# Performance work log

Measured on AMD Instinct MI355X. Metric: run time of the kernel, lower is better.

The kernel has to match this reference:

```python
import jax, jax.numpy as jnp
import numpy as np

N_USERS = 50000
N_PRODS = 50000
N_NODES = N_USERS + N_PRODS
N_EDGES = 600000
UD, PD, H, O = 64, 100, 128, 16


def _gcn_conv(x, W, b, src, dst, n):
    """PyG GCNConv: linear transform, add self-loops, sym-normalized scatter-add."""
    x = x @ W                                    # [n, H]
    loop = jnp.arange(n, dtype=src.dtype)
    src = jnp.concatenate([src, loop])
    dst = jnp.concatenate([dst, loop])
    deg = jax.ops.segment_sum(jnp.ones_like(dst, dtype=x.dtype), dst, num_segments=n)
    dinv = jnp.where(deg > 0, jax.lax.rsqrt(deg), 0.0)
    norm = dinv[src] * dinv[dst]                 # [E+n]
    msg = x[src] * norm[:, None]                 # gather + scale
    out = jax.ops.segment_sum(msg, dst, num_segments=n)
    return out + b


def setup_inputs() -> dict:
    key = jax.random.key(0)
    ks = jax.random.split(key, 16)
    s = 0.05
    return {
        "user_feats": jax.random.normal(ks[0], (N_USERS, UD), dtype=jnp.float32),
        "prod_feats": jax.random.normal(ks[1], (N_PRODS, PD), dtype=jnp.float32),
        "edge_index": jax.random.randint(ks[2], (2, N_EDGES), 0, N_NODES, dtype=jnp.int64),
        "Wu": jax.random.normal(ks[3], (UD, H), dtype=jnp.float32) * s,
        "bu": jnp.zeros((H,), dtype=jnp.float32),
        "Wp": jax.random.normal(ks[4], (PD, H), dtype=jnp.float32) * s,
        "bp": jnp.zeros((H,), dtype=jnp.float32),
        "W1": jax.random.normal(ks[5], (H, H), dtype=jnp.float32) * s,
        "b1": jnp.zeros((H,), dtype=jnp.float32),
        "W2": jax.random.normal(ks[6], (H, H), dtype=jnp.float32) * s,
        "b2": jnp.zeros((H,), dtype=jnp.float32),
        "W3": jax.random.normal(ks[7], (H, H), dtype=jnp.float32) * s,
        "b3": jnp.zeros((H,), dtype=jnp.float32),
        "Wo": jax.random.normal(ks[8], (H, O), dtype=jnp.float32) * s,
        "bo": jnp.zeros((O,), dtype=jnp.float32),
    }


def reference(user_feats, prod_feats, edge_index, Wu, bu, Wp, bp,
              W1, b1, W2, b2, W3, b3, Wo, bo):
    src, dst = edge_index[0], edge_index[1]
    user_x = user_feats @ Wu + bu
    prod_x = prod_feats @ Wp + bp
    x = jnp.concatenate([user_x, prod_x], axis=0)   # [N_NODES, H]
    x = jax.nn.relu(_gcn_conv(x, W1, b1, src, dst, N_NODES))
    # dropout p=0.6 is identity in eval mode
    x = jax.nn.relu(_gcn_conv(x, W2, b2, src, dst, N_NODES))
    x = jax.nn.relu(_gcn_conv(x, W3, b3, src, dst, N_NODES))
    return x @ Wo + bo                              # [N_NODES, O]
```

## Files before the change

### kernel.cpp

```cpp
#include <hip/hip_runtime.h>
#include <hip/hip_fp16.h>

#define NU 50000
#define NP 50000
#define NN 100000
#define NE 600000
#define H  128
#define O  16

typedef __attribute__((ext_vector_type(8))) _Float16 half8;
typedef __attribute__((ext_vector_type(4))) _Float16 h4v;
typedef __attribute__((ext_vector_type(4))) float f32x4;

__global__ void k_prep(const float* __restrict__ Wu, const float* __restrict__ Wp,
                       const float* __restrict__ W1, const float* __restrict__ W2,
                       const float* __restrict__ W3, const float* __restrict__ Wo,
                       __half* __restrict__ whU, __half* __restrict__ wlU,
                       __half* __restrict__ whP, __half* __restrict__ wlP,
                       __half* __restrict__ wh1, __half* __restrict__ wl1,
                       __half* __restrict__ wh2, __half* __restrict__ wl2,
                       __half* __restrict__ wh3, __half* __restrict__ wl3,
                       __half* __restrict__ whO, __half* __restrict__ wlO,
                       int* __restrict__ cnt) {
    int idx = blockIdx.x * blockDim.x + threadIdx.x;
    if (idx >= 75776) {
        int i = idx - 75776;
        if (i < NN) cnt[i] = 0;
        return;
    }
    const float* W; __half *Wh, *Wl; int K, KPAD, NC;
    if      (idx <  8192) {              W = Wu; Wh = whU; Wl = wlU; K =  64; KPAD =  64; NC = 128; }
    else if (idx < 24576) { idx -=  8192; W = Wp; Wh = whP; Wl = wlP; K = 100; KPAD = 128; NC = 128; }
    else if (idx < 40960) { idx -= 24576; W = W1; Wh = wh1; Wl = wl1; K = 128; KPAD = 128; NC = 128; }
    else if (idx < 57344) { idx -= 40960; W = W2; Wh = wh2; Wl = wl2; K = 128; KPAD = 128; NC = 128; }
    else if (idx < 73728) { idx -= 57344; W = W3; Wh = wh3; Wl = wl3; K = 128; KPAD = 128; NC = 128; }
    else                  { idx -= 73728; W = Wo; Wh = whO; Wl = wlO; K = 128; KPAD = 128; NC =  16; }
    int n = idx / KPAD, k = idx - n * KPAD;
    float x = (k < K) ? W[k * NC + n] * 16.0f : 0.0f;
    __half h = __float2half_rn(x);
    __half l = __float2half_rn(x - __half2float(h));
    Wh[idx] = h; Wl[idx] = l;
}

__global__ void k_count(const int* __restrict__ dst, int* __restrict__ cnt,
                        int* __restrict__ rank, int E) {
    int e = blockIdx.x * blockDim.x + threadIdx.x;
    if (e < E) rank[e] = atomicAdd(&cnt[dst[e]], 1);
}

#define SCAN_TPB 256
#define SCAN_VPT 4
#define SCAN_CHUNK (SCAN_TPB * SCAN_VPT)

__global__ void k_scan1(const int* __restrict__ in, int* __restrict__ out,
                        int* __restrict__ bsums, float* __restrict__ dinv, int n) {
    __shared__ int sh[SCAN_TPB];
    int t = threadIdx.x, b = blockIdx.x;
    int base = b * SCAN_CHUNK + t * SCAN_VPT;
    int v[SCAN_VPT]; int s = 0;
#pragma unroll
    for (int i = 0; i < SCAN_VPT; i++) {
        int idx = base + i;
        v[i] = (idx < n) ? in[idx] : 0;
        if (idx < n) dinv[idx] = rsqrtf((float)(v[i] + 1));
        s += v[i];
    }
    sh[t] = s; __syncthreads();
    for (int off = 1; off < SCAN_TPB; off <<= 1) {
        int x = (t >= off) ? sh[t - off] : 0;
        __syncthreads();
        sh[t] += x;
        __syncthreads();
    }
    int run = (t > 0) ? sh[t - 1] : 0;
    if (t == SCAN_TPB - 1) bsums[b] = sh[t];
#pragma unroll
    for (int i = 0; i < SCAN_VPT; i++) {
        int idx = base + i;
        if (idx < n) out[idx] = run;
        run += v[i];
    }
}

__global__ void k_scan2(int* __restrict__ bsums, int nb) {
    __shared__ int sh[128];
    int t = threadIdx.x;
    int v = (t < nb) ? bsums[t] : 0;
    sh[t] = v; __syncthreads();
    for (int off = 1; off < 128; off <<= 1) {
        int x = (t >= off) ? sh[t - off] : 0;
        __syncthreads();
        sh[t] += x;
        __syncthreads();
    }
    if (t < nb) bsums[t] = sh[t] - v;
}

__global__ void k_fill(const int* __restrict__ src, const int* __restrict__ dst,
                       const int* __restrict__ offs, const int* __restrict__ bsums,
                       const int* __restrict__ rank, const float* __restrict__ dinv,
                       int2* __restrict__ epack, int E) {
    int e = blockIdx.x * blockDim.x + threadIdx.x;
    if (e < E) {
        int s = src[e], d = dst[e];
        int p = offs[d] + bsums[d >> 10] + rank[e];
        int2 r;
        r.x = s;
        r.y = __float_as_int(dinv[s] * dinv[d]);
        epack[p] = r;
    }
}

template <typename AT, int K, int KPAD, int MI, int NOUT, bool BIAS, bool F32OUT>
__device__ __forceinline__
void gemm_body(const AT* __restrict__ X,
               const __half* __restrict__ Wh, const __half* __restrict__ Wl,
               const float* __restrict__ bias, void* __restrict__ Cout,
               int M, int orow0, int vb) {
    constexpr int KS = KPAD / 32;
    const int tid  = threadIdx.x;
    const int wid  = tid >> 6, lane = tid & 63;
    const int lm   = lane & 15, q = lane >> 4;
    const int gw   = vb * 4 + wid;
    const int NT   = (M + 63) >> 6;
    int tile, c0;
    if constexpr (MI == 4) { tile = gw >> 1; c0 = (gw & 1) * 64; }
    else                   { tile = gw;      c0 = 0; }
    if (tile >= NT) return;
    const int n0 = tile * 64;

    half8 wh[MI][KS], wl[MI][KS];
#pragma unroll
    for (int mi = 0; mi < MI; mi++)
#pragma unroll
        for (int ks = 0; ks < KS; ks++) {
            const size_t b = (size_t)(c0 + mi * 16 + lm) * KPAD + ks * 32 + q * 8;
            wh[mi][ks] = *(const half8*)&Wh[b];
            wl[mi][ks] = *(const half8*)&Wl[b];
        }

    f32x4 acc[4][MI];
#pragma unroll
    for (int ni = 0; ni < 4; ni++)
#pragma unroll
        for (int mi = 0; mi < MI; mi++) acc[ni][mi] = (f32x4)0.0f;

#pragma unroll
    for (int ni = 0; ni < 4; ni++) {
        const int node = n0 + ni * 16 + lm;
        half8 xf[KS];
        if (node < M) {
            if constexpr (sizeof(AT) == 2) {
#pragma unroll
                for (int ks = 0; ks < KS; ks++)
                    xf[ks] = *(const half8*)((const __half*)X + (size_t)node * KPAD + ks * 32 + q * 8);
            } else {
                const float* xp = (const float*)X + (size_t)node * K;
#pragma unroll
                for (int ks = 0; ks < KS; ks++) {
                    const int kb = ks * 32 + q * 8;
                    if (kb + 8 <= K) {
                        float4 v0 = *(const float4*)(xp + kb);
                        float4 v1 = *(const float4*)(xp + kb + 4);
                        xf[ks][0] = (_Float16)v0.x; xf[ks][1] = (_Float16)v0.y;
                        xf[ks][2] = (_Float16)v0.z; xf[ks][3] = (_Float16)v0.w;
                        xf[ks][4] = (_Float16)v1.x; xf[ks][5] = (_Float16)v1.y;
                        xf[ks][6] = (_Float16)v1.z; xf[ks][7] = (_Float16)v1.w;
                    } else {
#pragma unroll
                        for (int j = 0; j < 8; j++) {
                            int k = kb + j;
                            xf[ks][j] = (k < K) ? (_Float16)xp[k] : (_Float16)0.0f;
                        }
                    }
                }
            }
        } else {
#pragma unroll
            for (int ks = 0; ks < KS; ks++)
#pragma unroll
                for (int j = 0; j < 8; j++) xf[ks][j] = (_Float16)0.0f;
        }
#pragma unroll
        for (int ks = 0; ks < KS; ks++)
#pragma unroll
            for (int mi = 0; mi < MI; mi++) {
                acc[ni][mi] = __builtin_amdgcn_mfma_f32_16x16x32_f16(wh[mi][ks], xf[ks], acc[ni][mi], 0, 0, 0);
                acc[ni][mi] = __builtin_amdgcn_mfma_f32_16x16x32_f16(wl[mi][ks], xf[ks], acc[ni][mi], 0, 0, 0);
            }
    }

#pragma unroll
    for (int ni = 0; ni < 4; ni++) {
        const int node = n0 + ni * 16 + lm;
        if (node >= M) continue;
#pragma unroll
        for (int mi = 0; mi < MI; mi++) {
            const int cb = c0 + mi * 16 + q * 4;
            float4 bv = BIAS ? *(const float4*)&bias[cb] : make_float4(0.f, 0.f, 0.f, 0.f);
            float v0 = fmaf(acc[ni][mi][0], 0.0625f, bv.x);
            float v1 = fmaf(acc[ni][mi][1], 0.0625f, bv.y);
            float v2 = fmaf(acc[ni][mi][2], 0.0625f, bv.z);
            float v3 = fmaf(acc[ni][mi][3], 0.0625f, bv.w);
            if constexpr (F32OUT) {
                *(float4*)((float*)Cout + (size_t)(orow0 + node) * NOUT + cb) =
                    make_float4(v0, v1, v2, v3);
            } else {
                __half2 h0 = __floats2half2_rn(v0, v1);
                __half2 h1 = __floats2half2_rn(v2, v3);
                uint2 o; o.x = *(unsigned*)&h0; o.y = *(unsigned*)&h1;
                *(uint2*)((__half*)Cout + (size_t)(orow0 + node) * NOUT + cb) = o;
            }
        }
    }
}

template <typename AT, int K, int KPAD, int MI, int NOUT, bool BIAS, bool F32OUT>
__launch_bounds__(256)
__global__ void k_gemm_reg(const AT* __restrict__ X,
                           const __half* __restrict__ Wh, const __half* __restrict__ Wl,
                           const float* __restrict__ bias, void* __restrict__ Cout,
                           int M, int orow0) {
    gemm_body<AT, K, KPAD, MI, NOUT, BIAS, F32OUT>(X, Wh, Wl, bias, Cout, M, orow0, blockIdx.x);
}

__launch_bounds__(256)
__global__ void k_gemm_inputs(const float* __restrict__ user, const float* __restrict__ prod,
                              const __half* __restrict__ whU, const __half* __restrict__ wlU,
                              const __half* __restrict__ whP, const __half* __restrict__ wlP,
                              const float* __restrict__ bu, const float* __restrict__ bp,
                              void* __restrict__ xA, int blkU) {
    if ((int)blockIdx.x < blkU)
        gemm_body<float,  64,  64, 4, 128, true, false>(user, whU, wlU, bu, xA, NU, 0, blockIdx.x);
    else
        gemm_body<float, 100, 128, 4, 128, true, false>(prod, whP, wlP, bp, xA, NP, NU, blockIdx.x - blkU);
}

__launch_bounds__(256)
__global__ void k_aggregate(const __half* __restrict__ y, const int* __restrict__ offs,
                            const int* __restrict__ bsums, const int2* __restrict__ epack,
                            const float* __restrict__ dinv, const float* __restrict__ bias,
                            __half* __restrict__ out) {
    const int node = __builtin_amdgcn_readfirstlane(blockIdx.x * 4 + (threadIdx.x >> 6));
    const int l = threadIdx.x & 63;
    const int h = l >> 5, j = l & 31;

    int e0 = offs[node] + bsums[node >> 10];
    int e1 = (node + 1 < NN) ? (offs[node + 1] + bsums[(node + 1) >> 10]) : NE;
    e0 = __builtin_amdgcn_readfirstlane(e0);
    e1 = __builtin_amdgcn_readfirstlane(e1);

    const h4v* y4 = (const h4v*)y;
    f32x4 acc0 = (f32x4)0.f, acc1 = (f32x4)0.f, acc2 = (f32x4)0.f, acc3 = (f32x4)0.f;
    const int e1m1 = e1 - 1;

    for (int e = e0; e < e1; e += 8) {
        const int ee0 = e + 0 + h;
        const int ee1 = e + 2 + h;
        const int ee2 = e + 4 + h;
        const int ee3 = e + 6 + h;
        int2 p0 = epack[min(ee0, e1m1)];
        int2 p1 = epack[min(ee1, e1m1)];
        int2 p2 = epack[min(ee2, e1m1)];
        int2 p3 = epack[min(ee3, e1m1)];
        float w0 = (ee0 < e1) ? __int_as_float(p0.y) : 0.f;
        float w1 = (ee1 < e1) ? __int_as_float(p1.y) : 0.f;
        float w2 = (ee2 < e1) ? __int_as_float(p2.y) : 0.f;
        float w3 = (ee3 < e1) ? __int_as_float(p3.y) : 0.f;
        h4v v0 = y4[(size_t)p0.x * 32 + j];
        h4v v1 = y4[(size_t)p1.x * 32 + j];
        h4v v2 = y4[(size_t)p2.x * 32 + j];
        h4v v3 = y4[(size_t)p3.x * 32 + j];
        acc0[0] = fmaf((float)v0[0], w0, acc0[0]); acc0[1] = fmaf((float)v0[1], w0, acc0[1]);
        acc0[2] = fmaf((float)v0[2], w0, acc0[2]); acc0[3] = fmaf((float)v0[3], w0, acc0[3]);
        acc1[0] = fmaf((float)v1[0], w1, acc1[0]); acc1[1] = fmaf((float)v1[1], w1, acc1[1]);
        acc1[2] = fmaf((float)v1[2], w1, acc1[2]); acc1[3] = fmaf((float)v1[3], w1, acc1[3]);
        acc2[0] = fmaf((float)v2[0], w2, acc2[0]); acc2[1] = fmaf((float)v2[1], w2, acc2[1]);
        acc2[2] = fmaf((float)v2[2], w2, acc2[2]); acc2[3] = fmaf((float)v2[3], w2, acc2[3]);
        acc3[0] = fmaf((float)v3[0], w3, acc3[0]); acc3[1] = fmaf((float)v3[1], w3, acc3[1]);
        acc3[2] = fmaf((float)v3[2], w3, acc3[2]); acc3[3] = fmaf((float)v3[3], w3, acc3[3]);
    }

    f32x4 s = (acc0 + acc1) + (acc2 + acc3);
    float t0 = s[0] + __shfl_xor(s[0], 32, 64);
    float t1 = s[1] + __shfl_xor(s[1], 32, 64);
    float t2 = s[2] + __shfl_xor(s[2], 32, 64);
    float t3 = s[3] + __shfl_xor(s[3], 32, 64);

    const float di2 = dinv[node] * dinv[node];
    h4v sv = y4[(size_t)node * 32 + j];
    float4 bv = *(const float4*)&bias[4 * j];
    float r0 = fmaf((float)sv[0], di2, t0) + bv.x;
    float r1 = fmaf((float)sv[1], di2, t1) + bv.y;
    float r2 = fmaf((float)sv[2], di2, t2) + bv.z;
    float r3 = fmaf((float)sv[3], di2, t3) + bv.w;
    if (l < 32) {
        __half2 ha = __floats2half2_rn(fmaxf(r0, 0.f), fmaxf(r1, 0.f));
        __half2 hb = __floats2half2_rn(fmaxf(r2, 0.f), fmaxf(r3, 0.f));
        uint2 o; o.x = *(unsigned*)&ha; o.y = *(unsigned*)&hb;
        *(uint2*)(out + (size_t)node * H + 4 * j) = o;
    }
}

extern "C" void kernel_launch(void* const* d_in, const int* in_sizes, int n_in,
                              void* d_out, int out_size, void* d_ws, size_t ws_size,
                              hipStream_t stream) {
    const float* user = (const float*)d_in[0];
    const float* prod = (const float*)d_in[1];
    const int*   eidx = (const int*)  d_in[2];
    const int*   edst = eidx + NE;
    const int*   esrc = eidx;
    const float* Wu = (const float*)d_in[3];
    const float* bu = (const float*)d_in[4];
    const float* Wp = (const float*)d_in[5];
    const float* bp = (const float*)d_in[6];
    const float* W1 = (const float*)d_in[7];
    const float* b1 = (const float*)d_in[8];
    const float* W2 = (const float*)d_in[9];
    const float* b2 = (const float*)d_in[10];
    const float* W3 = (const float*)d_in[11];
    const float* b3 = (const float*)d_in[12];
    const float* Wo = (const float*)d_in[13];
    const float* bo = (const float*)d_in[14];
    float* out = (float*)d_out;

    char* ws = (char*)d_ws;
    size_t p = 0;
    auto alloc = [&](size_t bytes) -> void* {
        void* r = ws + p;
        p += (bytes + 255) & ~(size_t)255;
        return r;
    };
    __half* xA   = (__half*)alloc((size_t)NN * H * 2);
    __half* xB   = (__half*)alloc((size_t)NN * H * 2);
    int*   cnt   = (int*)  alloc((size_t)NN * 4);
    int*   rank  = (int*)  alloc((size_t)NE * 4);
    int*   offs  = (int*)  alloc((size_t)(NN + 1) * 4);
    float* dinv  = (float*)alloc((size_t)NN * 4);
    int2*  epack = (int2*) alloc((size_t)NE * 8);
    int*   bsums = (int*)  alloc(128 * 4);
    __half* whU = (__half*)alloc(128 * 64 * 2);
    __half* wlU = (__half*)alloc(128 * 64 * 2);
    __half* whP = (__half*)alloc(128 * 128 * 2);
    __half* wlP = (__half*)alloc(128 * 128 * 2);
    __half* wh1 = (__half*)alloc(128 * 128 * 2);
    __half* wl1 = (__half*)alloc(128 * 128 * 2);
    __half* wh2 = (__half*)alloc(128 * 128 * 2);
    __half* wl2 = (__half*)alloc(128 * 128 * 2);
    __half* wh3 = (__half*)alloc(128 * 128 * 2);
    __half* wl3 = (__half*)alloc(128 * 128 * 2);
    __half* whO = (__half*)alloc(16 * 128 * 2);
    __half* wlO = (__half*)alloc(16 * 128 * 2);

    const int NBLK = (NN + SCAN_CHUNK - 1) / SCAN_CHUNK;

    k_prep<<<(75776 + NN + 255) / 256, 256, 0, stream>>>(
        Wu, Wp, W1, W2, W3, Wo,
        whU, wlU, whP, wlP, wh1, wl1, wh2, wl2, wh3, wl3, whO, wlO, cnt);

    k_count<<<(NE + 255) / 256, 256, 0, stream>>>(edst, cnt, rank, NE);
    k_scan1<<<NBLK, SCAN_TPB, 0, stream>>>(cnt, offs, bsums, dinv, NN);
    k_scan2<<<1, 128, 0, stream>>>(bsums, NBLK);
    k_fill <<<(NE + 255) / 256, 256, 0, stream>>>(esrc, edst, offs, bsums, rank, dinv,
                                                  epack, NE);

    {
        constexpr int ntU = (NU + 63) / 64, blkU = (ntU * 2 + 3) / 4;
        constexpr int ntP = (NP + 63) / 64, blkP = (ntP * 2 + 3) / 4;
        k_gemm_inputs<<<blkU + blkP, 256, 0, stream>>>(
            user, prod, whU, wlU, whP, wlP, bu, bp, xA, blkU);
    }

    const int ntN  = (NN + 63) / 64;
    const int blkG = (ntN * 2 + 3) / 4;
    const int blkO = (ntN + 3) / 4;

    k_gemm_reg<__half, 128, 128, 4, 128, false, false><<<blkG, 256, 0, stream>>>(xA, wh1, wl1, nullptr, xB, NN, 0);
    k_aggregate<<<NN / 4, 256, 0, stream>>>(xB, offs, bsums, epack, dinv, b1, xA);
    k_gemm_reg<__half, 128, 128, 4, 128, false, false><<<blkG, 256, 0, stream>>>(xA, wh2, wl2, nullptr, xB, NN, 0);
    k_aggregate<<<NN / 4, 256, 0, stream>>>(xB, offs, bsums, epack, dinv, b2, xA);
    k_gemm_reg<__half, 128, 128, 4, 128, false, false><<<blkG, 256, 0, stream>>>(xA, wh3, wl3, nullptr, xB, NN, 0);
    k_aggregate<<<NN / 4, 256, 0, stream>>>(xB, offs, bsums, epack, dinv, b3, xA);

    k_gemm_reg<__half, 128, 128, 1, 16, true, true><<<blkO, 256, 0, stream>>>(xA, whO, wlO, bo, out, NN, 0);
}
```

Baseline: 303.2 us.

## Shrink GEMM tiles to 16 nodes per wave and vectorize aggregate edge loads

The register GEMM now gives each wave 16 nodes instead of 64. Weights are reloaded per k-step from cache rather than held in registers for the whole tile. This cuts register pressure and raises the number of waves in flight, at the cost of more weight loads from L1/L2. The aggregate kernel reads 4 contiguous packed edges per half-wave instead of strided clamped indices. It relies on an 8-entry zero-padded tail in the edge array, initialized in the prep kernel. The self-term and bias loads are hoisted before the edge loop so they overlap with the gathers.

```diff
diff --git a/kernel.cpp b/kernel.cpp
--- a/kernel.cpp
+++ b/kernel.cpp
@@ -21,11 +21,12 @@
                        __half* __restrict__ wh2, __half* __restrict__ wl2,
                        __half* __restrict__ wh3, __half* __restrict__ wl3,
                        __half* __restrict__ whO, __half* __restrict__ wlO,
-                       int* __restrict__ cnt) {
+                       int* __restrict__ cnt, int2* __restrict__ epack) {
     int idx = blockIdx.x * blockDim.x + threadIdx.x;
     if (idx >= 75776) {
         int i = idx - 75776;
         if (i < NN) cnt[i] = 0;
+        else if (i < NN + 8) { int2 z; z.x = 0; z.y = 0; epack[NE + (i - NN)] = z; }
         return;
     }
     const float* W; __half *Wh, *Wl; int K, KPAD, NC;
@@ -118,99 +119,87 @@
                const float* __restrict__ bias, void* __restrict__ Cout,
                int M, int orow0, int vb) {
     constexpr int KS = KPAD / 32;
+    constexpr int CSPLIT = NOUT / (16 * MI);
     const int tid  = threadIdx.x;
     const int wid  = tid >> 6, lane = tid & 63;
     const int lm   = lane & 15, q = lane >> 4;
     const int gw   = vb * 4 + wid;
-    const int NT   = (M + 63) >> 6;
-    int tile, c0;
-    if constexpr (MI == 4) { tile = gw >> 1; c0 = (gw & 1) * 64; }
-    else                   { tile = gw;      c0 = 0; }
-    if (tile >= NT) return;
-    const int n0 = tile * 64;
-
-    half8 wh[MI][KS], wl[MI][KS];
-#pragma unroll
-    for (int mi = 0; mi < MI; mi++)
-#pragma unroll
-        for (int ks = 0; ks < KS; ks++) {
-            const size_t b = (size_t)(c0 + mi * 16 + lm) * KPAD + ks * 32 + q * 8;
-            wh[mi][ks] = *(const half8*)&Wh[b];
-            wl[mi][ks] = *(const half8*)&Wl[b];
-        }
-
-    f32x4 acc[4][MI];
-#pragma unroll
-    for (int ni = 0; ni < 4; ni++)
-#pragma unroll
-        for (int mi = 0; mi < MI; mi++) acc[ni][mi] = (f32x4)0.0f;
-
-#pragma unroll
-    for (int ni = 0; ni < 4; ni++) {
-        const int node = n0 + ni * 16 + lm;
-        half8 xf[KS];
-        if (node < M) {
-            if constexpr (sizeof(AT) == 2) {
-#pragma unroll
-                for (int ks = 0; ks < KS; ks++)
-                    xf[ks] = *(const half8*)((const __half*)X + (size_t)node * KPAD + ks * 32 + q * 8);
-            } else {
-                const float* xp = (const float*)X + (size_t)node * K;
-#pragma unroll
-                for (int ks = 0; ks < KS; ks++) {
-                    const int kb = ks * 32 + q * 8;
-                    if (kb + 8 <= K) {
-                        float4 v0 = *(const float4*)(xp + kb);
-                        float4 v1 = *(const float4*)(xp + kb + 4);
-                        xf[ks][0] = (_Float16)v0.x; xf[ks][1] = (_Float16)v0.y;
-                        xf[ks][2] = (_Float16)v0.z; xf[ks][3] = (_Float16)v0.w;
-                        xf[ks][4] = (_Float16)v1.x; xf[ks][5] = (_Float16)v1.y;
-                        xf[ks][6] = (_Float16)v1.z; xf[ks][7] = (_Float16)v1.w;
-                    } else {
-#pragma unroll
-                        for (int j = 0; j < 8; j++) {
-                            int k = kb + j;
-                            xf[ks][j] = (k < K) ? (_Float16)xp[k] : (_Float16)0.0f;
-                        }
-                    }
+    const int ng   = gw / CSPLIT;
+    const int c0   = (gw % CSPLIT) * (MI * 16);
+    const int NT16 = (M + 15) >> 4;
+    if (ng >= NT16) return;
+    const int node = ng * 16 + lm;
+
+    half8 xf[KS];
+    if (node < M) {
+        if constexpr (sizeof(AT) == 2) {
+#pragma unroll
+            for (int ks = 0; ks < KS; ks++)
+                xf[ks] = *(const half8*)((const __half*)X + (size_t)node * KPAD + ks * 32 + q * 8);
+        } else {
+            const float* xp = (const float*)X + (size_t)node * K;
+#pragma unroll
+            for (int ks = 0; ks < KS; ks++) {
+                const int kb = ks * 32 + q * 8;
+                if (kb + 8 <= K) {
+                    float4 v0 = *(const float4*)(xp + kb);
+                    float4 v1 = *(const float4*)(xp + kb + 4);
+                    xf[ks][0] = (_Float16)v0.x; xf[ks][1] = (_Float16)v0.y;
+                    xf[ks][2] = (_Float16)v0.z; xf[ks][3] = (_Float16)v0.w;
+                    xf[ks][4] = (_Float16)v1.x; xf[ks][5] = (_Float16)v1.y;
+                    xf[ks][6] = (_Float16)v1.z; xf[ks][7] = (_Float16)v1.w;
+                } else if (kb + 4 <= K) {
+                    float4 v0 = *(const float4*)(xp + kb);
+                    xf[ks][0] = (_Float16)v0.x; xf[ks][1] = (_Float16)v0.y;
+                    xf[ks][2] = (_Float16)v0.z; xf[ks][3] = (_Float16)v0.w;
+                    xf[ks][4] = (_Float16)0.0f; xf[ks][5] = (_Float16)0.0f;
+                    xf[ks][6] = (_Float16)0.0f; xf[ks][7] = (_Float16)0.0f;
+                } else {
+#pragma unroll
+                    for (int j = 0; j < 8; j++) xf[ks][j] = (_Float16)0.0f;
                 }
             }
+        }
+    } else {
+#pragma unroll
+        for (int ks = 0; ks < KS; ks++)
+#pragma unroll
+            for (int j = 0; j < 8; j++) xf[ks][j] = (_Float16)0.0f;
+    }
+
+    f32x4 acc[MI];
+#pragma unroll
+    for (int mi = 0; mi < MI; mi++) acc[mi] = (f32x4)0.0f;
+
+#pragma unroll
+    for (int ks = 0; ks < KS; ks++) {
+#pragma unroll
+        for (int mi = 0; mi < MI; mi++) {
+            const size_t b = (size_t)(c0 + mi * 16 + lm) * KPAD + ks * 32 + q * 8;
+            half8 wh = *(const half8*)&Wh[b];
+            half8 wl = *(const half8*)&Wl[b];
+            acc[mi] = __builtin_amdgcn_mfma_f32_16x16x32_f16(wh, xf[ks], acc[mi], 0, 0, 0);
+            acc[mi] = __builtin_amdgcn_mfma_f32_16x16x32_f16(wl, xf[ks], acc[mi], 0, 0, 0);
+        }
+    }
+
+    if (node >= M) return;
+#pragma unroll
+    for (int mi = 0; mi < MI; mi++) {
+        const int cb = c0 + mi * 16 + q * 4;
+        float4 bv = BIAS ? *(const float4*)&bias[cb] : make_float4(0.f, 0.f, 0.f, 0.f);
+        float v0 = fmaf(acc[mi][0], 0.0625f, bv.x);
+        float v1 = fmaf(acc[mi][1], 0.0625f, bv.y);
+        float v2 = fmaf(acc[mi][2], 0.0625f, bv.z);
+        float v3 = fmaf(acc[mi][3], 0.0625f, bv.w);
+        if constexpr (F32OUT) {
+            *(float4*)((float*)Cout + (size_t)(orow0 + node) * NOUT + cb) =
+                make_float4(v0, v1, v2, v3);
         } else {
-#pragma unroll
-            for (int ks = 0; ks < KS; ks++)
-#pragma unroll
-                for (int j = 0; j < 8; j++) xf[ks][j] = (_Float16)0.0f;
-        }
-#pragma unroll
-        for (int ks = 0; ks < KS; ks++)
-#pragma unroll
-            for (int mi = 0; mi < MI; mi++) {
-                acc[ni][mi] = __builtin_amdgcn_mfma_f32_16x16x32_f16(wh[mi][ks], xf[ks], acc[ni][mi], 0, 0, 0);
-                acc[ni][mi] = __builtin_amdgcn_mfma_f32_16x16x32_f16(wl[mi][ks], xf[ks], acc[ni][mi], 0, 0, 0);
-            }
-    }
-
-#pragma unroll
-    for (int ni = 0; ni < 4; ni++) {
-        const int node = n0 + ni * 16 + lm;
-        if (node >= M) continue;
-#pragma unroll
-        for (int mi = 0; mi < MI; mi++) {
-            const int cb = c0 + mi * 16 + q * 4;
-            float4 bv = BIAS ? *(const float4*)&bias[cb] : make_float4(0.f, 0.f, 0.f, 0.f);
-            float v0 = fmaf(acc[ni][mi][0], 0.0625f, bv.x);
-            float v1 = fmaf(acc[ni][mi][1], 0.0625f, bv.y);
-            float v2 = fmaf(acc[ni][mi][2], 0.0625f, bv.z);
-            float v3 = fmaf(acc[ni][mi][3], 0.0625f, bv.w);
-            if constexpr (F32OUT) {
-                *(float4*)((float*)Cout + (size_t)(orow0 + node) * NOUT + cb) =
-                    make_float4(v0, v1, v2, v3);
-            } else {
-                __half2 h0 = __floats2half2_rn(v0, v1);
-                __half2 h1 = __floats2half2_rn(v2, v3);
-                uint2 o; o.x = *(unsigned*)&h0; o.y = *(unsigned*)&h1;
-                *(uint2*)((__half*)Cout + (size_t)(orow0 + node) * NOUT + cb) = o;
-            }
+            __half2 h0 = __floats2half2_rn(v0, v1);
+            __half2 h1 = __floats2half2_rn(v2, v3);
+            uint2 o; o.x = *(unsigned*)&h0; o.y = *(unsigned*)&h1;
+            *(uint2*)((__half*)Cout + (size_t)(orow0 + node) * NOUT + cb) = o;
         }
     }
 }
@@ -251,22 +240,24 @@
     e1 = __builtin_amdgcn_readfirstlane(e1);
 
     const h4v* y4 = (const h4v*)y;
+
+    const float di2 = dinv[node] * dinv[node];
+    h4v sv = y4[(size_t)node * 32 + j];
+    float4 bv = *(const float4*)&bias[4 * j];
+
     f32x4 acc0 = (f32x4)0.f, acc1 = (f32x4)0.f, acc2 = (f32x4)0.f, acc3 = (f32x4)0.f;
-    const int e1m1 = e1 - 1;
 
     for (int e = e0; e < e1; e += 8) {
-        const int ee0 = e + 0 + h;
-        const int ee1 = e + 2 + h;
-        const int ee2 = e + 4 + h;
-        const int ee3 = e + 6 + h;
-        int2 p0 = epack[min(ee0, e1m1)];
-        int2 p1 = epack[min(ee1, e1m1)];
-        int2 p2 = epack[min(ee2, e1m1)];
-        int2 p3 = epack[min(ee3, e1m1)];
-        float w0 = (ee0 < e1) ? __int_as_float(p0.y) : 0.f;
-        float w1 = (ee1 < e1) ? __int_as_float(p1.y) : 0.f;
-        float w2 = (ee2 < e1) ? __int_as_float(p2.y) : 0.f;
-        float w3 = (ee3 < e1) ? __int_as_float(p3.y) : 0.f;
+        const int eb = e + 4 * h;
+        const int2* pe = epack + eb;
+        int2 p0 = pe[0];
+        int2 p1 = pe[1];
+        int2 p2 = pe[2];
+        int2 p3 = pe[3];
+        float w0 = (eb + 0 < e1) ? __int_as_float(p0.y) : 0.f;
+        float w1 = (eb + 1 < e1) ? __int_as_float(p1.y) : 0.f;
+        float w2 = (eb + 2 < e1) ? __int_as_float(p2.y) : 0.f;
+        float w3 = (eb + 3 < e1) ? __int_as_float(p3.y) : 0.f;
         h4v v0 = y4[(size_t)p0.x * 32 + j];
         h4v v1 = y4[(size_t)p1.x * 32 + j];
         h4v v2 = y4[(size_t)p2.x * 32 + j];
@@ -287,9 +278,6 @@
     float t2 = s[2] + __shfl_xor(s[2], 32, 64);
     float t3 = s[3] + __shfl_xor(s[3], 32, 64);
 
-    const float di2 = dinv[node] * dinv[node];
-    h4v sv = y4[(size_t)node * 32 + j];
-    float4 bv = *(const float4*)&bias[4 * j];
     float r0 = fmaf((float)sv[0], di2, t0) + bv.x;
     float r1 = fmaf((float)sv[1], di2, t1) + bv.y;
     float r2 = fmaf((float)sv[2], di2, t2) + bv.z;
@@ -337,7 +325,7 @@
     int*   rank  = (int*)  alloc((size_t)NE * 4);
     int*   offs  = (int*)  alloc((size_t)(NN + 1) * 4);
     float* dinv  = (float*)alloc((size_t)NN * 4);
-    int2*  epack = (int2*) alloc((size_t)NE * 8);
+    int2*  epack = (int2*) alloc((size_t)(NE + 8) * 8);
     int*   bsums = (int*)  alloc(128 * 4);
     __half* whU = (__half*)alloc(128 * 64 * 2);
     __half* wlU = (__half*)alloc(128 * 64 * 2);
@@ -354,9 +342,9 @@
 
     const int NBLK = (NN + SCAN_CHUNK - 1) / SCAN_CHUNK;
 
-    k_prep<<<(75776 + NN + 255) / 256, 256, 0, stream>>>(
+    k_prep<<<(75776 + NN + 8 + 255) / 256, 256, 0, stream>>>(
         Wu, Wp, W1, W2, W3, Wo,
-        whU, wlU, whP, wlP, wh1, wl1, wh2, wl2, wh3, wl3, whO, wlO, cnt);
+        whU, wlU, whP, wlP, wh1, wl1, wh2, wl2, wh3, wl3, whO, wlO, cnt, epack);
 
     k_count<<<(NE + 255) / 256, 256, 0, stream>>>(edst, cnt, rank, NE);
     k_scan1<<<NBLK, SCAN_TPB, 0, stream>>>(cnt, offs, bsums, dinv, NN);
@@ -365,15 +353,14 @@
                                                   epack, NE);
 
     {
-        constexpr int ntU = (NU + 63) / 64, blkU = (ntU * 2 + 3) / 4;
-        constexpr int ntP = (NP + 63) / 64, blkP = (ntP * 2 + 3) / 4;
+        constexpr int blkU = (3125 * 2 + 3) / 4;
+        constexpr int blkP = (3125 * 2 + 3) / 4;
         k_gemm_inputs<<<blkU + blkP, 256, 0, stream>>>(
             user, prod, whU, wlU, whP, wlP, bu, bp, xA, blkU);
     }
 
-    const int ntN  = (NN + 63) / 64;
-    const int blkG = (ntN * 2 + 3) / 4;
-    const int blkO = (ntN + 3) / 4;
+    const int blkG = (6250 * 2 + 3) / 4;
+    const int blkO = (6250 + 3) / 4;
 
     k_gemm_reg<__half, 128, 128, 4, 128, false, false><<<blkG, 256, 0, stream>>>(xA, wh1, wl1, nullptr, xB, NN, 0);
     k_aggregate<<<NN / 4, 256, 0, stream>>>(xB, offs, bsums, epack, dinv, b1, xA);
```

Result: slower. 393.2 us (+29.7%).
